# Kernel optimization log

Measured on AMD Instinct MI355X. Metric: run time of the kernel, lower is better.

The kernel has to match this reference:

```python
import jax, jax.numpy as jnp
import numpy as np

NC = 80
CENTER_RADIUS = 2.5
TOPK = 10
BOX_W, CLS_W, OBJ_W = 7.5, 0.5, 1.0
ALPHA, GAMMA = 0.25, 2.0
EPS = 1e-7
BIG = 1e10


def _corners(b):
    x, y, w, h = b[..., 0], b[..., 1], b[..., 2], b[..., 3]
    return x - w / 2, y - h / 2, x + w / 2, y + h / 2


def _pairwise_iou(b1, b2):
    # b1: (N,4) xywh, b2: (G,4) xywh -> (N,G) plain IoU
    x11, y11, x12, y12 = [t[:, None] for t in _corners(b1)]
    x21, y21, x22, y22 = _corners(b2)
    inter = jnp.clip(jnp.minimum(x12, x22) - jnp.maximum(x11, x21), 0) * \
            jnp.clip(jnp.minimum(y12, y22) - jnp.maximum(y11, y21), 0)
    union = (b1[:, 2] * b1[:, 3])[:, None] + (b2[:, 2] * b2[:, 3])[None, :] - inter + EPS
    return inter / union


def _ciou(b1, b2):
    # aligned boxes (N,4),(N,4) xywh -> (N,) CIoU
    x11, y11, x12, y12 = _corners(b1)
    x21, y21, x22, y22 = _corners(b2)
    w1, h1 = b1[..., 2], b1[..., 3]
    w2, h2 = b2[..., 2], b2[..., 3]
    inter = jnp.clip(jnp.minimum(x12, x22) - jnp.maximum(x11, x21), 0) * \
            jnp.clip(jnp.minimum(y12, y22) - jnp.maximum(y11, y21), 0)
    union = w1 * h1 + w2 * h2 - inter + EPS
    iou = inter / union
    cw = jnp.maximum(x12, x22) - jnp.minimum(x11, x21)
    ch = jnp.maximum(y12, y22) - jnp.minimum(y11, y21)
    c2 = cw ** 2 + ch ** 2 + EPS
    rho2 = ((x11 + x12 - x21 - x22) ** 2 + (y11 + y12 - y21 - y22) ** 2) / 4
    v = (4.0 / jnp.pi ** 2) * (jnp.arctan(w2 / (h2 + EPS)) - jnp.arctan(w1 / (h1 + EPS))) ** 2
    alpha = jax.lax.stop_gradient(v / (v - iou + (1.0 + EPS)))
    return iou - (rho2 / c2 + v * alpha)


def _assign(pred_boxes, pred_scores, gt_boxes, gt_classes, anchor_centers):
    # SimOTA: returns fg mask (N,) bool and matched gt index per anchor (N,)
    N = pred_boxes.shape[0]
    G = gt_boxes.shape[0]
    d = jnp.sqrt(jnp.sum((anchor_centers[:, None, :] - gt_boxes[None, :, :2]) ** 2, -1))
    cand = (d < CENTER_RADIUS).any(axis=1)                      # (N,) center prior
    cand = jnp.where(cand.any(), cand, jnp.ones_like(cand))     # fallback: all anchors
    n_cand = cand.sum().astype(jnp.int32)
    iou = _pairwise_iou(pred_boxes, gt_boxes)                   # (N,G)
    iou = jnp.where(cand[:, None], iou, 0.0)                    # candidates only
    iou_cost = -jnp.log(iou + 1e-8)
    # cls cost: BCE-with-logits of sigmoid scores vs one-hot gt, summed over classes.
    # sum_c bce(s_c, y_c) = sum_c softplus(s_c) - s_{gt}; avoids (N,G,nc) tensor.
    sp_sum = jax.nn.softplus(pred_scores).sum(axis=1)           # (N,)
    cls_cost = sp_sum[:, None] - pred_scores[:, gt_classes]     # (N,G)
    cost = jnp.where(cand[:, None], iou_cost + 3.0 * cls_cost, BIG)
    # dynamic-k: k_j = clip(floor(sum_i iou[i,j]), 1, min(topk, n_cand))
    dyn_k = jnp.maximum(jnp.floor(iou.sum(axis=0)).astype(jnp.int32), 1)
    dyn_k = jnp.minimum(dyn_k, jnp.minimum(TOPK, n_cand))       # (G,)
    _, topk_idx = jax.lax.top_k(-cost.T, TOPK)                  # (G,TOPK) smallest-cost anchors
    keep = jnp.arange(TOPK)[None, :] < dyn_k[:, None]           # (G,TOPK)
    matching = jnp.zeros((G, N), dtype=bool).at[jnp.arange(G)[:, None], topk_idx].set(keep)
    matching = matching.T                                       # (N,G)
    # conflict resolution: anchors matched to >1 gt keep only min-cost gt
    count = matching.sum(axis=1)
    best = jnp.argmin(jnp.where(matching, cost, BIG), axis=1)
    matching = jnp.where((count > 1)[:, None], jax.nn.one_hot(best, G, dtype=bool), matching)
    fg = matching.any(axis=1)
    matched_gt = jnp.argmax(matching, axis=1)
    return fg, matched_gt


def _image_loss(pred, gt_boxes, gt_classes, anchor_centers):
    pb = pred[:, :4]
    pc = pred[:, 4:4 + NC]
    po = pred[:, -1]
    fg, mgt = _assign(pb, jax.nn.sigmoid(pc), gt_boxes, gt_classes, anchor_centers)
    fg_f = fg.astype(pred.dtype)
    # objectness: BCE-with-logits, mean over anchors
    obj = (jax.nn.softplus(po) - po * fg_f).mean()
    # box: CIoU on matched pairs (masked sum)
    tgt_boxes = gt_boxes[mgt]                                   # (N,4)
    box = jnp.sum((1.0 - _ciou(pb, tgt_boxes)) * fg_f)
    # cls: focal BCE on matched anchors
    tgt_cls = jax.nn.one_hot(gt_classes[mgt], NC, dtype=pred.dtype)
    bce = jax.nn.softplus(pc) - pc * tgt_cls
    p = jax.nn.sigmoid(pc)
    p_t = p * tgt_cls + (1 - p) * (1 - tgt_cls)
    cls = jnp.sum((ALPHA * (1 - p_t) ** GAMMA * bce).sum(axis=1) * fg_f)
    return box, cls, obj, fg_f.sum()


def setup_inputs() -> dict:
    B, N, M = 4, 33600, 100
    key = jax.random.key(0)
    ks = jax.random.split(key, 7)
    boxes_xy = jax.random.uniform(ks[0], (B, N, 2)) * 640.0
    boxes_wh = jax.random.uniform(ks[1], (B, N, 2)) * 100.0 + 10.0
    logits = jax.random.normal(ks[2], (B, N, NC + 1))
    pred = jnp.concatenate([boxes_xy, boxes_wh, logits], axis=-1)    # (B,N,85)
    gt_xy = jax.random.uniform(ks[3], (B, M, 2)) * 640.0
    gt_wh = jax.random.uniform(ks[4], (B, M, 2)) * 100.0 + 10.0
    gt_boxes = jnp.concatenate([gt_xy, gt_wh], axis=-1)              # (B,M,4), all valid (sum>0)
    gt_classes = jax.random.randint(ks[5], (B, M), 0, NC, dtype=jnp.int32)
    anchor_centers = jax.random.uniform(ks[6], (N, 2)) * 640.0
    return {"pred": pred, "gt_boxes": gt_boxes, "gt_classes": gt_classes,
            "anchor_centers": anchor_centers}


def reference(pred, gt_boxes, gt_classes, anchor_centers):
    box, cls, obj, npos = jax.vmap(_image_loss, in_axes=(0, 0, 0, None))(
        pred, gt_boxes, gt_classes, anchor_centers)
    n_pos = jnp.maximum(npos.sum(), 1.0)
    total = BOX_W * box.sum() / n_pos + CLS_W * cls.sum() / n_pos + OBJ_W * obj.sum()
    return total
```

## Files before the change

kernel.cpp:

```cpp
#include <hip/hip_runtime.h>
#include <math.h>

#define B_ 4
#define N_ 33600
#define G_ 100
#define NCLS 80
#define STRIDE 85
#define TK 10
#define K1BLK 132
#define K4BLK 525

__device__ __forceinline__ float sigmoidf_(float x) {
    return 1.0f / (1.0f + expf(-x));
}
__device__ __forceinline__ float softplusf_(float x) {
    return fmaxf(x, 0.0f) + log1pf(expf(-fabsf(x)));
}
__device__ __forceinline__ float waveRedSum(float v) {
    #pragma unroll
    for (int off = 32; off; off >>= 1) v += __shfl_xor(v, off, 64);
    return v;
}
__device__ __forceinline__ int waveRedSumI(int v) {
    #pragma unroll
    for (int off = 32; off; off >>= 1) v += __shfl_xor(v, off, 64);
    return v;
}

__global__ void k1_prep(const float* __restrict__ gtb,
                        const float* __restrict__ anc,
                        const float* __restrict__ pred,
                        unsigned char* __restrict__ mask,
                        float* __restrict__ spsum,
                        unsigned long long* __restrict__ bkey,
                        float* __restrict__ pobj,
                        int* __restrict__ bcount,
                        unsigned int* __restrict__ done)
{
    __shared__ float gcx[G_], gcy[G_];
    const int b = blockIdx.y;
    const int tid = threadIdx.x;
    const int lane = tid & 63, wid = tid >> 6;
    if (blockIdx.x == 0 && b == 0 && tid == 0) *done = 0u;
    if (tid < G_) {
        gcx[tid] = gtb[(b * G_ + tid) * 4 + 0];
        gcy[tid] = gtb[(b * G_ + tid) * 4 + 1];
    }
    __syncthreads();
    const int n = blockIdx.x * blockDim.x + tid;
    float so = 0.0f;
    int c = 0;
    if (n < N_) {
        const size_t a_ = (size_t)b * N_ + n;
        bkey[a_] = 0xFFFFFFFFFFFFFFFFull;
        so = softplusf_(pred[a_ * STRIDE + (STRIDE - 1)]);
        const float2 a = ((const float2*)anc)[n];
        #pragma unroll 10
        for (int g = 0; g < G_; ++g) {
            const float dx = a.x - gcx[g], dy = a.y - gcy[g];
            c |= (dx * dx + dy * dy < 6.25f) ? 1 : 0;
        }
        mask[a_] = (unsigned char)c;
        unsigned long long m = __ballot(c != 0);
        while (m) {
            const int src = (int)__ffsll(m) - 1;
            m &= (m - 1);
            const int an = __shfl(n, src, 64);
            const float* row = pred + ((size_t)b * N_ + an) * STRIDE + 4;
            float s = softplusf_(sigmoidf_(row[lane]));
            if (lane < NCLS - 64) s += softplusf_(sigmoidf_(row[64 + lane]));
            s = waveRedSum(s);
            if (lane == 0) spsum[(size_t)b * N_ + an] = s;
        }
    }
    so = waveRedSum(so);
    const int wc = waveRedSumI(c);
    __shared__ float wsf[4];
    __shared__ int wci[4];
    if (lane == 0) { wsf[wid] = so; wci[wid] = wc; }
    __syncthreads();
    if (tid == 0) {
        pobj[b * K1BLK + blockIdx.x] = wsf[0] + wsf[1] + wsf[2] + wsf[3];
        bcount[b * K1BLK + blockIdx.x] = wci[0] + wci[1] + wci[2] + wci[3];
    }
}

__global__ void k2_scatter(const unsigned char* __restrict__ mask,
                           const int* __restrict__ bcount,
                           int* __restrict__ cidx,
                           int* __restrict__ counts)
{
    const int b = blockIdx.y;
    const int blk = blockIdx.x;
    const int tid = threadIdx.x;
    const int lane = tid & 63, wid = tid >> 6;

    __shared__ int red[256];
    const int v = (tid < K1BLK) ? bcount[b * K1BLK + tid] : 0;

    red[tid] = (tid < blk) ? v : 0;
    __syncthreads();
    for (int s = 128; s > 0; s >>= 1) {
        if (tid < s) red[tid] += red[tid + s];
        __syncthreads();
    }
    const int base = red[0];
    __syncthreads();

    if (blk == 0) {
        red[tid] = v;
        __syncthreads();
        for (int s = 128; s > 0; s >>= 1) {
            if (tid < s) red[tid] += red[tid + s];
            __syncthreads();
        }
        if (tid == 0) {
            counts[b * 2 + 0] = red[0];
            counts[b * 2 + 1] = (red[0] == 0) ? 1 : 0;
        }
        __syncthreads();
    }

    const int n = blk * 256 + tid;
    const int c = (n < N_) ? (int)mask[(size_t)b * N_ + n] : 0;
    int incl = c;
    #pragma unroll
    for (int off = 1; off < 64; off <<= 1) {
        const int t = __shfl_up(incl, off, 64);
        if (lane >= off) incl += t;
    }
    __shared__ int wsum[4];
    if (lane == 63) wsum[wid] = incl;
    __syncthreads();
    int wbase = 0;
    for (int w = 0; w < wid; ++w) wbase += wsum[w];
    if (c) cidx[(size_t)b * N_ + base + wbase + incl - 1] = n;
}

__global__ void __launch_bounds__(64)
k3_topk(const float* __restrict__ pred,
        const float* __restrict__ gtb,
        const int* __restrict__ gtc,
        const int* __restrict__ cidx,
        const int* __restrict__ counts,
        const float* __restrict__ spsum,
        unsigned long long* __restrict__ bkey)
{
    const int b = blockIdx.y, g = blockIdx.x;
    const int lane = threadIdx.x;
    const int cnt = counts[b * 2 + 0];
    const int allc = counts[b * 2 + 1];
    const int count = allc ? N_ : cnt;

    const float* gb = gtb + (b * G_ + g) * 4;
    const float gxc = gb[0], gyc = gb[1], gw = gb[2], gh = gb[3];
    const float gx1 = gxc - gw * 0.5f, gy1 = gyc - gh * 0.5f;
    const float gx2 = gxc + gw * 0.5f, gy2 = gyc + gh * 0.5f;
    const float garea = gw * gh;
    const int cls = gtc[b * G_ + g];

    float kcost[TK];
    int   kslot[TK];
    #pragma unroll
    for (int j = 0; j < TK; ++j) { kcost[j] = INFINITY; kslot[j] = 0x7FFFFFFF; }

    float iousum = 0.0f;
    for (int i = lane; i < count; i += 64) {
        const int n = allc ? i : cidx[(size_t)b * N_ + i];
        const float* pr = pred + (size_t)(b * N_ + n) * STRIDE;
        const float px = pr[0], py = pr[1], pw = pr[2], ph = pr[3];
        const float x1 = px - pw * 0.5f, y1 = py - ph * 0.5f;
        const float x2 = px + pw * 0.5f, y2 = py + ph * 0.5f;
        float sp;
        if (allc) {
            float s = 0.0f;
            for (int cc = 0; cc < NCLS; ++cc) s += softplusf_(sigmoidf_(pr[4 + cc]));
            sp = s;
        } else {
            sp = spsum[(size_t)b * N_ + n];
        }
        const float iw = fmaxf(fminf(x2, gx2) - fmaxf(x1, gx1), 0.0f);
        const float ih = fmaxf(fminf(y2, gy2) - fmaxf(y1, gy1), 0.0f);
        const float inter = iw * ih;
        const float uni = pw * ph + garea - inter + 1e-7f;
        const float iou = inter / uni;
        iousum += iou;
        const float sgc = sigmoidf_(pr[4 + cls]);
        float c = -logf(iou + 1e-8f) + 3.0f * (sp - sgc);
        int   s = i;
        #pragma unroll
        for (int j = 0; j < TK; ++j) {
            const bool lt = (c < kcost[j]);
            const float tc = kcost[j]; const int ts = kslot[j];
            if (lt) { kcost[j] = c; kslot[j] = s; c = tc; s = ts; }
        }
    }

    #pragma unroll
    for (int off = 32; off; off >>= 1) iousum += __shfl_xor(iousum, off, 64);

    unsigned long long win[TK];
    #pragma unroll
    for (int r = 0; r < TK; ++r) {
        const unsigned long long mykey =
            ((unsigned long long)__float_as_uint(kcost[0]) << 32) | (unsigned)kslot[0];
        unsigned long long k2 = mykey;
        #pragma unroll
        for (int off = 32; off; off >>= 1) {
            const unsigned long long o = __shfl_xor(k2, off, 64);
            k2 = (o < k2) ? o : k2;
        }
        win[r] = k2;
        if (mykey == k2) {
            #pragma unroll
            for (int j = 0; j < TK - 1; ++j) { kcost[j] = kcost[j + 1]; kslot[j] = kslot[j + 1]; }
            kcost[TK - 1] = INFINITY; kslot[TK - 1] = 0x7FFFFFFF;
        }
    }

    const int kmax = (count < TK) ? count : TK;
    int dk = (int)floorf(iousum);
    if (dk < 1) dk = 1;
    if (dk > kmax) dk = kmax;

    if (lane == 0) {
        #pragma unroll
        for (int r = 0; r < TK; ++r) {
            if (r < dk) {
                const unsigned slot = (unsigned)(win[r] & 0xFFFFFFFFull);
                const int n = allc ? (int)slot : cidx[(size_t)b * N_ + (int)slot];
                const unsigned cbits = (unsigned)(win[r] >> 32);
                const unsigned long long key =
                    ((unsigned long long)cbits << 32) | (unsigned)g;
                atomicMin(&bkey[(size_t)b * N_ + n], key);
            }
        }
    }
}

__global__ void k4_fg(const float* __restrict__ pred,
                      const float* __restrict__ gtb,
                      const int* __restrict__ gtc,
                      const unsigned long long* __restrict__ bkey,
                      const float* __restrict__ pobj,
                      float* __restrict__ pfg,
                      unsigned int* __restrict__ done,
                      float* __restrict__ out)
{
    const int tid = threadIdx.x;
    const unsigned i = blockIdx.x * blockDim.x + tid;
    const int lane = tid & 63, wid = tid >> 6;
    const unsigned long long key = bkey[i];
    const bool fg = (key != 0xFFFFFFFFFFFFFFFFull);
    float posum = 0.0f, box = 0.0f, clsacc = 0.0f, npos = 0.0f;

    unsigned long long m = __ballot(fg);
    while (m) {
        const int src = (int)__ffsll(m) - 1;
        m &= (m - 1);
        const unsigned ai = (unsigned)__shfl((int)i, src, 64);
        const int mg = __shfl((int)(unsigned)(key & 0xFFFFFFFFull), src, 64);
        const int b = (int)(ai / (unsigned)N_);
        const float* pr = pred + (size_t)ai * STRIDE;
        const int cg_ = gtc[b * G_ + mg];
        {
            const float x = pr[4 + lane];
            const float t = (lane == cg_) ? 1.0f : 0.0f;
            const float bce = softplusf_(x) - x * t;
            const float p = sigmoidf_(x);
            const float pt = t * p + (1.0f - t) * (1.0f - p);
            const float om = 1.0f - pt;
            clsacc += 0.25f * om * om * bce;
        }
        if (lane < NCLS - 64) {
            const float x = pr[4 + 64 + lane];
            const float t = ((64 + lane) == cg_) ? 1.0f : 0.0f;
            const float bce = softplusf_(x) - x * t;
            const float p = sigmoidf_(x);
            const float pt = t * p + (1.0f - t) * (1.0f - p);
            const float om = 1.0f - pt;
            clsacc += 0.25f * om * om * bce;
        }
        if (lane == 0) {
            npos += 1.0f;
            posum += pr[STRIDE - 1];
            const float* gb = gtb + (b * G_ + mg) * 4;
            const float px = pr[0], py = pr[1], pw = pr[2], ph = pr[3];
            const float gx = gb[0], gy = gb[1], gw = gb[2], gh = gb[3];
            const float x11 = px - pw * 0.5f, y11 = py - ph * 0.5f;
            const float x12 = px + pw * 0.5f, y12 = py + ph * 0.5f;
            const float x21 = gx - gw * 0.5f, y21 = gy - gh * 0.5f;
            const float x22 = gx + gw * 0.5f, y22 = gy + gh * 0.5f;
            const float iw = fmaxf(fminf(x12, x22) - fmaxf(x11, x21), 0.0f);
            const float ih = fmaxf(fminf(y12, y22) - fmaxf(y11, y21), 0.0f);
            const float inter = iw * ih;
            const float uni = pw * ph + gw * gh - inter + 1e-7f;
            const float iou = inter / uni;
            const float cw = fmaxf(x12, x22) - fminf(x11, x21);
            const float chh = fmaxf(y12, y22) - fminf(y11, y21);
            const float c2 = cw * cw + chh * chh + 1e-7f;
            const float ddx = x11 + x12 - x21 - x22;
            const float ddy = y11 + y12 - y21 - y22;
            const float rho2 = (ddx * ddx + ddy * ddy) * 0.25f;
            const float dv = atanf(gw / (gh + 1e-7f)) - atanf(pw / (ph + 1e-7f));
            const float v = (float)(4.0 / (M_PI * M_PI)) * dv * dv;
            const float alpha = v / (v - iou + 1.0f + 1e-7f);
            const float ciou = iou - (rho2 / c2 + v * alpha);
            box += 1.0f - ciou;
        }
    }

    posum = waveRedSum(posum);
    box = waveRedSum(box);
    clsacc = waveRedSum(clsacc);
    npos = waveRedSum(npos);
    __shared__ float ws[4][4];
    if (lane == 0) {
        ws[wid][0] = posum; ws[wid][1] = box;
        ws[wid][2] = clsacc; ws[wid][3] = npos;
    }
    __syncthreads();
    __shared__ int amlast;
    if (tid == 0) {
        float* p = pfg + (size_t)blockIdx.x * 4;
        #pragma unroll
        for (int k = 0; k < 4; ++k) {
            const float v = ws[0][k] + ws[1][k] + ws[2][k] + ws[3][k];
            __hip_atomic_store(&p[k], v, __ATOMIC_RELAXED, __HIP_MEMORY_SCOPE_AGENT);
        }
        const unsigned prev = __hip_atomic_fetch_add(done, 1u, __ATOMIC_ACQ_REL,
                                                     __HIP_MEMORY_SCOPE_AGENT);
        amlast = (prev == (unsigned)(K4BLK - 1)) ? 1 : 0;
    }
    __syncthreads();
    if (!amlast) return;

    float so = 0, sp = 0, sb = 0, sc = 0, sn = 0;
    for (int k = tid; k < B_ * K1BLK; k += 256) so += pobj[k];
    for (int k = tid; k < K4BLK; k += 256) {
        const float* p = pfg + (size_t)k * 4;
        sp += __hip_atomic_load(&p[0], __ATOMIC_RELAXED, __HIP_MEMORY_SCOPE_AGENT);
        sb += __hip_atomic_load(&p[1], __ATOMIC_RELAXED, __HIP_MEMORY_SCOPE_AGENT);
        sc += __hip_atomic_load(&p[2], __ATOMIC_RELAXED, __HIP_MEMORY_SCOPE_AGENT);
        sn += __hip_atomic_load(&p[3], __ATOMIC_RELAXED, __HIP_MEMORY_SCOPE_AGENT);
    }
    __shared__ float red[256];
    float in5[5] = {so, sp, sb, sc, sn};
    float res[5];
    #pragma unroll
    for (int k = 0; k < 5; ++k) {
        red[tid] = in5[k];
        __syncthreads();
        for (int s = 128; s > 0; s >>= 1) {
            if (tid < s) red[tid] += red[tid + s];
            __syncthreads();
        }
        res[k] = red[0];
        __syncthreads();
    }
    if (tid == 0) {
        const float obj_sum = res[0] - res[1];
        const float n_pos = fmaxf(res[4], 1.0f);
        out[0] = 7.5f * res[2] / n_pos
               + 0.5f * res[3] / n_pos
               + obj_sum / (float)N_;
    }
}

extern "C" void kernel_launch(void* const* d_in, const int* in_sizes, int n_in,
                              void* d_out, int out_size, void* d_ws, size_t ws_size,
                              hipStream_t stream)
{
    const float* pred = (const float*)d_in[0];
    const float* gtb  = (const float*)d_in[1];
    const int*   gtc  = (const int*)d_in[2];
    const float* anc  = (const float*)d_in[3];

    char* ws = (char*)d_ws;
    size_t off = 0;
    auto take = [&](size_t bytes) {
        size_t o = off;
        off += (bytes + 255) & ~(size_t)255;
        return o;
    };
    unsigned char*      mask   = (unsigned char*)(ws + take((size_t)B_ * N_));
    int*                cidx   = (int*)(ws + take((size_t)B_ * N_ * 4));
    int*                counts = (int*)(ws + take((size_t)B_ * 2 * 4));
    unsigned long long* bkey   = (unsigned long long*)(ws + take((size_t)B_ * N_ * 8));
    float*              spsum  = (float*)(ws + take((size_t)B_ * N_ * 4));
    float*              pobj   = (float*)(ws + take((size_t)B_ * K1BLK * 4));
    int*                bcount = (int*)(ws + take((size_t)B_ * K1BLK * 4));
    float*              pfg    = (float*)(ws + take((size_t)K4BLK * 4 * 4));
    unsigned int*       done   = (unsigned int*)(ws + take(4));

    dim3 g1(K1BLK, B_);
    k1_prep<<<g1, 256, 0, stream>>>(gtb, anc, pred, mask, spsum, bkey, pobj,
                                    bcount, done);
    dim3 g2(K1BLK, B_);
    k2_scatter<<<g2, 256, 0, stream>>>(mask, bcount, cidx, counts);
    dim3 g3(G_, B_);
    k3_topk<<<g3, 64, 0, stream>>>(pred, gtb, gtc, cidx, counts, spsum, bkey);
    k4_fg<<<K4BLK, 256, 0, stream>>>(pred, gtb, gtc, bkey, pobj, pfg, done,
                                     (float*)d_out);
}
```

Baseline: 43.55 us.

## Fuse candidate compaction into prep and widen top-k blocks to 256 threads

Removes the separate scatter kernel. k1 now writes per-block compacted candidate indices into a padded buffer and records per-block counts. The top-k kernel runs a prefix scan over those block counts and gathers candidate indices into shared memory in chunks. It also uses four waves per ground-truth box instead of one, merging per-wave top-10 lists through shared memory. This saves a launch and increases parallelism in the top-k scan, at the cost of a redundant 256-wide scan in every block and a serial per-thread gather loop.

```diff
diff --git a/kernel.cpp b/kernel.cpp
--- a/kernel.cpp
+++ b/kernel.cpp
@@ -8,7 +8,9 @@
 #define STRIDE 85
 #define TK 10
 #define K1BLK 132
-#define K4BLK 525
+#define K3BLK 525
+#define CAP 2048
+#define PADW (K1BLK * 256)
 
 __device__ __forceinline__ float sigmoidf_(float x) {
     return 1.0f / (1.0f + expf(-x));
@@ -17,11 +19,6 @@
     return fmaxf(x, 0.0f) + log1pf(expf(-fabsf(x)));
 }
 __device__ __forceinline__ float waveRedSum(float v) {
-    #pragma unroll
-    for (int off = 32; off; off >>= 1) v += __shfl_xor(v, off, 64);
-    return v;
-}
-__device__ __forceinline__ int waveRedSumI(int v) {
     #pragma unroll
     for (int off = 32; off; off >>= 1) v += __shfl_xor(v, off, 64);
     return v;
@@ -30,7 +27,7 @@
 __global__ void k1_prep(const float* __restrict__ gtb,
                         const float* __restrict__ anc,
                         const float* __restrict__ pred,
-                        unsigned char* __restrict__ mask,
+                        int* __restrict__ cidx_pad,
                         float* __restrict__ spsum,
                         unsigned long long* __restrict__ bkey,
                         float* __restrict__ pobj,
@@ -38,6 +35,8 @@
                         unsigned int* __restrict__ done)
 {
     __shared__ float gcx[G_], gcy[G_];
+    __shared__ int wsum[4];
+    __shared__ float wsf[4];
     const int b = blockIdx.y;
     const int tid = threadIdx.x;
     const int lane = tid & 63, wid = tid >> 6;
@@ -60,7 +59,6 @@
             const float dx = a.x - gcx[g], dy = a.y - gcy[g];
             c |= (dx * dx + dy * dy < 6.25f) ? 1 : 0;
         }
-        mask[a_] = (unsigned char)c;
         unsigned long long m = __ballot(c != 0);
         while (m) {
             const int src = (int)__ffsll(m) - 1;
@@ -73,84 +71,57 @@
             if (lane == 0) spsum[(size_t)b * N_ + an] = s;
         }
     }
-    so = waveRedSum(so);
-    const int wc = waveRedSumI(c);
-    __shared__ float wsf[4];
-    __shared__ int wci[4];
-    if (lane == 0) { wsf[wid] = so; wci[wid] = wc; }
-    __syncthreads();
-    if (tid == 0) {
-        pobj[b * K1BLK + blockIdx.x] = wsf[0] + wsf[1] + wsf[2] + wsf[3];
-        bcount[b * K1BLK + blockIdx.x] = wci[0] + wci[1] + wci[2] + wci[3];
-    }
-}
-
-__global__ void k2_scatter(const unsigned char* __restrict__ mask,
-                           const int* __restrict__ bcount,
-                           int* __restrict__ cidx,
-                           int* __restrict__ counts)
-{
-    const int b = blockIdx.y;
-    const int blk = blockIdx.x;
-    const int tid = threadIdx.x;
-    const int lane = tid & 63, wid = tid >> 6;
-
-    __shared__ int red[256];
-    const int v = (tid < K1BLK) ? bcount[b * K1BLK + tid] : 0;
-
-    red[tid] = (tid < blk) ? v : 0;
-    __syncthreads();
-    for (int s = 128; s > 0; s >>= 1) {
-        if (tid < s) red[tid] += red[tid + s];
-        __syncthreads();
-    }
-    const int base = red[0];
-    __syncthreads();
-
-    if (blk == 0) {
-        red[tid] = v;
-        __syncthreads();
-        for (int s = 128; s > 0; s >>= 1) {
-            if (tid < s) red[tid] += red[tid + s];
-            __syncthreads();
-        }
-        if (tid == 0) {
-            counts[b * 2 + 0] = red[0];
-            counts[b * 2 + 1] = (red[0] == 0) ? 1 : 0;
-        }
-        __syncthreads();
-    }
-
-    const int n = blk * 256 + tid;
-    const int c = (n < N_) ? (int)mask[(size_t)b * N_ + n] : 0;
     int incl = c;
     #pragma unroll
     for (int off = 1; off < 64; off <<= 1) {
         const int t = __shfl_up(incl, off, 64);
         if (lane >= off) incl += t;
     }
-    __shared__ int wsum[4];
     if (lane == 63) wsum[wid] = incl;
+    const float sow = waveRedSum(so);
+    if (lane == 0) wsf[wid] = sow;
     __syncthreads();
     int wbase = 0;
     for (int w = 0; w < wid; ++w) wbase += wsum[w];
-    if (c) cidx[(size_t)b * N_ + base + wbase + incl - 1] = n;
-}
-
-__global__ void __launch_bounds__(64)
-k3_topk(const float* __restrict__ pred,
+    if (c) cidx_pad[(size_t)b * PADW + blockIdx.x * 256 + wbase + incl - 1] = n;
+    if (tid == 0) {
+        pobj[b * K1BLK + blockIdx.x] = wsf[0] + wsf[1] + wsf[2] + wsf[3];
+        bcount[b * K1BLK + blockIdx.x] = wsum[0] + wsum[1] + wsum[2] + wsum[3];
+    }
+}
+
+__global__ void __launch_bounds__(256)
+k2_topk(const float* __restrict__ pred,
         const float* __restrict__ gtb,
         const int* __restrict__ gtc,
-        const int* __restrict__ cidx,
-        const int* __restrict__ counts,
+        const int* __restrict__ cidx_pad,
+        const int* __restrict__ bcount,
         const float* __restrict__ spsum,
         unsigned long long* __restrict__ bkey)
 {
     const int b = blockIdx.y, g = blockIdx.x;
-    const int lane = threadIdx.x;
-    const int cnt = counts[b * 2 + 0];
-    const int allc = counts[b * 2 + 1];
+    const int tid = threadIdx.x;
+    const int lane = tid & 63, wid = tid >> 6;
+
+    __shared__ int scan[256];
+    __shared__ int clds[CAP];
+    __shared__ unsigned long long warr[4][TK];
+    __shared__ float iolds[4];
+
+    const int myc = (tid < K1BLK) ? bcount[b * K1BLK + tid] : 0;
+    scan[tid] = myc;
+    __syncthreads();
+    #pragma unroll
+    for (int off = 1; off < 256; off <<= 1) {
+        const int v = (tid >= off) ? scan[tid - off] : 0;
+        __syncthreads();
+        scan[tid] += v;
+        __syncthreads();
+    }
+    const int cnt = scan[K1BLK - 1];
+    const int allc = (cnt == 0) ? 1 : 0;
     const int count = allc ? N_ : cnt;
+    const int ebase = (tid == 0) ? 0 : scan[tid - 1];
 
     const float* gb = gtb + (b * G_ + g) * 4;
     const float gxc = gb[0], gyc = gb[1], gw = gb[2], gh = gb[3];
@@ -160,85 +131,115 @@
     const int cls = gtc[b * G_ + g];
 
     float kcost[TK];
-    int   kslot[TK];
-    #pragma unroll
-    for (int j = 0; j < TK; ++j) { kcost[j] = INFINITY; kslot[j] = 0x7FFFFFFF; }
-
+    int   kid[TK];
+    #pragma unroll
+    for (int j = 0; j < TK; ++j) { kcost[j] = INFINITY; kid[j] = 0x7FFFFFFF; }
     float iousum = 0.0f;
-    for (int i = lane; i < count; i += 64) {
-        const int n = allc ? i : cidx[(size_t)b * N_ + i];
-        const float* pr = pred + (size_t)(b * N_ + n) * STRIDE;
-        const float px = pr[0], py = pr[1], pw = pr[2], ph = pr[3];
-        const float x1 = px - pw * 0.5f, y1 = py - ph * 0.5f;
-        const float x2 = px + pw * 0.5f, y2 = py + ph * 0.5f;
-        float sp;
-        if (allc) {
-            float s = 0.0f;
-            for (int cc = 0; cc < NCLS; ++cc) s += softplusf_(sigmoidf_(pr[4 + cc]));
-            sp = s;
-        } else {
-            sp = spsum[(size_t)b * N_ + n];
-        }
-        const float iw = fmaxf(fminf(x2, gx2) - fmaxf(x1, gx1), 0.0f);
-        const float ih = fmaxf(fminf(y2, gy2) - fmaxf(y1, gy1), 0.0f);
-        const float inter = iw * ih;
-        const float uni = pw * ph + garea - inter + 1e-7f;
-        const float iou = inter / uni;
-        iousum += iou;
-        const float sgc = sigmoidf_(pr[4 + cls]);
-        float c = -logf(iou + 1e-8f) + 3.0f * (sp - sgc);
-        int   s = i;
-        #pragma unroll
-        for (int j = 0; j < TK; ++j) {
-            const bool lt = (c < kcost[j]);
-            const float tc = kcost[j]; const int ts = kslot[j];
-            if (lt) { kcost[j] = c; kslot[j] = s; c = tc; s = ts; }
-        }
-    }
-
-    #pragma unroll
-    for (int off = 32; off; off >>= 1) iousum += __shfl_xor(iousum, off, 64);
-
-    unsigned long long win[TK];
+
+    for (int lo = 0; lo < count; lo += CAP) {
+        const int hi = (count < lo + CAP) ? count : (lo + CAP);
+        if (!allc && tid < K1BLK && myc) {
+            for (int j = 0; j < myc; ++j) {
+                const int d = ebase + j;
+                if (d >= lo && d < hi)
+                    clds[d - lo] = cidx_pad[(size_t)b * PADW + tid * 256 + j];
+            }
+        }
+        __syncthreads();
+        for (int i = lo + tid; i < hi; i += 256) {
+            int n;
+            float sp;
+            if (allc) {
+                n = i;
+                const float* pr0 = pred + (size_t)(b * N_ + n) * STRIDE;
+                float s = 0.0f;
+                for (int cc = 0; cc < NCLS; ++cc) s += softplusf_(sigmoidf_(pr0[4 + cc]));
+                sp = s;
+            } else {
+                n = clds[i - lo];
+                sp = spsum[(size_t)b * N_ + n];
+            }
+            const float* pr = pred + (size_t)(b * N_ + n) * STRIDE;
+            const float px = pr[0], py = pr[1], pw = pr[2], ph = pr[3];
+            const float x1 = px - pw * 0.5f, y1 = py - ph * 0.5f;
+            const float x2 = px + pw * 0.5f, y2 = py + ph * 0.5f;
+            const float iw = fmaxf(fminf(x2, gx2) - fmaxf(x1, gx1), 0.0f);
+            const float ih = fmaxf(fminf(y2, gy2) - fmaxf(y1, gy1), 0.0f);
+            const float inter = iw * ih;
+            const float uni = pw * ph + garea - inter + 1e-7f;
+            const float iou = inter / uni;
+            iousum += iou;
+            const float sgc = sigmoidf_(pr[4 + cls]);
+            float c = -logf(iou + 1e-8f) + 3.0f * (sp - sgc);
+            int   s = n;
+            #pragma unroll
+            for (int j = 0; j < TK; ++j) {
+                const bool lt = (c < kcost[j]);
+                const float tc = kcost[j]; const int ts = kid[j];
+                if (lt) { kcost[j] = c; kid[j] = s; c = tc; s = ts; }
+            }
+        }
+        __syncthreads();
+    }
+
+    const float ios = waveRedSum(iousum);
+    if (lane == 0) iolds[wid] = ios;
+
     #pragma unroll
     for (int r = 0; r < TK; ++r) {
         const unsigned long long mykey =
-            ((unsigned long long)__float_as_uint(kcost[0]) << 32) | (unsigned)kslot[0];
+            ((unsigned long long)__float_as_uint(kcost[0]) << 32) | (unsigned)kid[0];
         unsigned long long k2 = mykey;
         #pragma unroll
         for (int off = 32; off; off >>= 1) {
             const unsigned long long o = __shfl_xor(k2, off, 64);
             k2 = (o < k2) ? o : k2;
         }
-        win[r] = k2;
+        if (lane == 0) warr[wid][r] = k2;
         if (mykey == k2) {
             #pragma unroll
-            for (int j = 0; j < TK - 1; ++j) { kcost[j] = kcost[j + 1]; kslot[j] = kslot[j + 1]; }
-            kcost[TK - 1] = INFINITY; kslot[TK - 1] = 0x7FFFFFFF;
-        }
-    }
-
-    const int kmax = (count < TK) ? count : TK;
-    int dk = (int)floorf(iousum);
-    if (dk < 1) dk = 1;
-    if (dk > kmax) dk = kmax;
-
-    if (lane == 0) {
+            for (int j = 0; j < TK - 1; ++j) { kcost[j] = kcost[j + 1]; kid[j] = kid[j + 1]; }
+            kcost[TK - 1] = INFINITY; kid[TK - 1] = 0x7FFFFFFF;
+        }
+    }
+    __syncthreads();
+
+    if (wid == 0) {
+        unsigned long long key = 0xFFFFFFFFFFFFFFFFull;
+        if (lane < 4 * TK) key = warr[lane / TK][lane % TK];
+        unsigned long long win[TK];
         #pragma unroll
         for (int r = 0; r < TK; ++r) {
-            if (r < dk) {
-                const unsigned slot = (unsigned)(win[r] & 0xFFFFFFFFull);
-                const int n = allc ? (int)slot : cidx[(size_t)b * N_ + (int)slot];
-                const unsigned cbits = (unsigned)(win[r] >> 32);
-                const unsigned long long key =
-                    ((unsigned long long)cbits << 32) | (unsigned)g;
-                atomicMin(&bkey[(size_t)b * N_ + n], key);
+            unsigned long long k2 = key;
+            #pragma unroll
+            for (int off = 32; off; off >>= 1) {
+                const unsigned long long o = __shfl_xor(k2, off, 64);
+                k2 = (o < k2) ? o : k2;
             }
-        }
-    }
-}
-
-__global__ void k4_fg(const float* __restrict__ pred,
+            win[r] = k2;
+            if (key == k2) key = 0xFFFFFFFFFFFFFFFFull;
+        }
+        const float total_iou = iolds[0] + iolds[1] + iolds[2] + iolds[3];
+        const int kmax = (count < TK) ? count : TK;
+        int dk = (int)floorf(total_iou);
+        if (dk < 1) dk = 1;
+        if (dk > kmax) dk = kmax;
+        if (lane == 0) {
+            #pragma unroll
+            for (int r = 0; r < TK; ++r) {
+                if (r < dk) {
+                    const int n = (int)(unsigned)(win[r] & 0xFFFFFFFFull);
+                    const unsigned cbits = (unsigned)(win[r] >> 32);
+                    const unsigned long long key2 =
+                        ((unsigned long long)cbits << 32) | (unsigned)g;
+                    atomicMin(&bkey[(size_t)b * N_ + n], key2);
+                }
+            }
+        }
+    }
+}
+
+__global__ void k3_fg(const float* __restrict__ pred,
                       const float* __restrict__ gtb,
                       const int* __restrict__ gtc,
                       const unsigned long long* __restrict__ bkey,
@@ -330,14 +331,14 @@
         }
         const unsigned prev = __hip_atomic_fetch_add(done, 1u, __ATOMIC_ACQ_REL,
                                                      __HIP_MEMORY_SCOPE_AGENT);
-        amlast = (prev == (unsigned)(K4BLK - 1)) ? 1 : 0;
+        amlast = (prev == (unsigned)(K3BLK - 1)) ? 1 : 0;
     }
     __syncthreads();
     if (!amlast) return;
 
     float so = 0, sp = 0, sb = 0, sc = 0, sn = 0;
     for (int k = tid; k < B_ * K1BLK; k += 256) so += pobj[k];
-    for (int k = tid; k < K4BLK; k += 256) {
+    for (int k = tid; k < K3BLK; k += 256) {
         const float* p = pfg + (size_t)k * 4;
         sp += __hip_atomic_load(&p[0], __ATOMIC_RELAXED, __HIP_MEMORY_SCOPE_AGENT);
         sb += __hip_atomic_load(&p[1], __ATOMIC_RELAXED, __HIP_MEMORY_SCOPE_AGENT);
@@ -383,23 +384,19 @@
         off += (bytes + 255) & ~(size_t)255;
         return o;
     };
-    unsigned char*      mask   = (unsigned char*)(ws + take((size_t)B_ * N_));
-    int*                cidx   = (int*)(ws + take((size_t)B_ * N_ * 4));
-    int*                counts = (int*)(ws + take((size_t)B_ * 2 * 4));
-    unsigned long long* bkey   = (unsigned long long*)(ws + take((size_t)B_ * N_ * 8));
-    float*              spsum  = (float*)(ws + take((size_t)B_ * N_ * 4));
-    float*              pobj   = (float*)(ws + take((size_t)B_ * K1BLK * 4));
-    int*                bcount = (int*)(ws + take((size_t)B_ * K1BLK * 4));
-    float*              pfg    = (float*)(ws + take((size_t)K4BLK * 4 * 4));
-    unsigned int*       done   = (unsigned int*)(ws + take(4));
+    int*                cidx_pad = (int*)(ws + take((size_t)B_ * PADW * 4));
+    unsigned long long* bkey     = (unsigned long long*)(ws + take((size_t)B_ * N_ * 8));
+    float*              spsum    = (float*)(ws + take((size_t)B_ * N_ * 4));
+    float*              pobj     = (float*)(ws + take((size_t)B_ * K1BLK * 4));
+    int*                bcount   = (int*)(ws + take((size_t)B_ * K1BLK * 4));
+    float*              pfg      = (float*)(ws + take((size_t)K3BLK * 4 * 4));
+    unsigned int*       done     = (unsigned int*)(ws + take(4));
 
     dim3 g1(K1BLK, B_);
-    k1_prep<<<g1, 256, 0, stream>>>(gtb, anc, pred, mask, spsum, bkey, pobj,
-                                    bcount, done);
-    dim3 g2(K1BLK, B_);
-    k2_scatter<<<g2, 256, 0, stream>>>(mask, bcount, cidx, counts);
-    dim3 g3(G_, B_);
-    k3_topk<<<g3, 64, 0, stream>>>(pred, gtb, gtc, cidx, counts, spsum, bkey);
-    k4_fg<<<K4BLK, 256, 0, stream>>>(pred, gtb, gtc, bkey, pobj, pfg, done,
+    k1_prep<<<g1, 256, 0, stream>>>(gtb, anc, pred, cidx_pad, spsum, bkey,
+                                    pobj, bcount, done);
+    dim3 g2(G_, B_);
+    k2_topk<<<g2, 256, 0, stream>>>(pred, gtb, gtc, cidx_pad, bcount, spsum, bkey);
+    k3_fg<<<K3BLK, 256, 0, stream>>>(pred, gtb, gtc, bkey, pobj, pfg, done,
                                      (float*)d_out);
 }
```

Result: faster. 41.52 us (-4.7%).
